# Kernel tuning notes

Measured on AMD Instinct MI355X. Metric: run time of the kernel, lower is better.

## Reference

```python
import jax, jax.numpy as jnp
import numpy as np

BETA = 0.25


def setup_inputs() -> dict:
    key = jax.random.key(0)
    k1, k2 = jax.random.split(key)
    z_e = jax.random.normal(k1, (16, 256, 2048), dtype=jnp.float32)   # [B, C, L]
    # nn.Embedding weight initialized uniform(-1, 1): [num_codewords, codebook_dim]
    emb = jax.random.uniform(k2, (2048, 256), dtype=jnp.float32, minval=-1.0, maxval=1.0)
    return {"z_e": z_e, "emb": emb}


def reference(z_e, emb):
    C = emb.shape[1]
    # Faithful to the torch code: permute(2,1,0) -> [L, C, B], then view(-1, C)
    z = jnp.transpose(z_e, (2, 1, 0))          # [L, C, B]
    flat = z.reshape(-1, C)                    # [N, C] where N = L*C*B / C
    d = (jnp.sum(flat * flat, axis=1, keepdims=True)
         + jnp.sum(emb * emb, axis=1)
         - 2.0 * flat @ emb.T)                 # [N, K]
    indices = jnp.argmin(d, axis=1)            # [N]
    quantized = emb[indices].reshape(z.shape)  # [L, C, B]
    sg = jax.lax.stop_gradient
    vq_loss = (jnp.mean((sg(quantized) - z) ** 2)
               + BETA * jnp.mean((quantized - sg(z)) ** 2))
    return quantized, indices, vq_loss
```

## Files before the change

### kernel.cpp

```cpp
#include <hip/hip_runtime.h>


#define ZE_CL   (256 * 2048)
#define NROWS   32768
#define KC      2048
#define DD      256
#define IDX_OFF 8388608
#define LOSS_OFF (8388608 + 32768)
#define D2 8e-3f

typedef __bf16 bf16x4 __attribute__((ext_vector_type(4)));
typedef __bf16 bf16x8 __attribute__((ext_vector_type(8)));
typedef float  f32x4  __attribute__((ext_vector_type(4)));

#define EN_OFF  0u
#define EH_OFF  8192u
#define EL_OFF  (EH_OFF + 1048576u)
#define AH_OFF  (EL_OFF + 1048576u)
#define AL_OFF  (AH_OFF + 16777216u)
#define CNT_OFF (AL_OFF + 16777216u)
#define LST_OFF (CNT_OFF + 16u)
#define WS_NEED (LST_OFF + 131072u)

static __device__ inline void gld_lds16(const void* g, void* l) {
    __builtin_amdgcn_global_load_lds(
        (const __attribute__((address_space(1))) void*)g,
        (__attribute__((address_space(3))) void*)l, 16, 0, 0);
}

__global__ void vq_prep_emb(const float* __restrict__ emb, float* __restrict__ enorm,
                            __bf16* __restrict__ Eh, __bf16* __restrict__ El) {
    int col = blockIdx.x * 256 + threadIdx.x;
    const float4* src = (const float4*)(emb + (size_t)col * DD);
    int t8 = col >> 8, g = (col >> 4) & 15, c = col & 15;
    float s = 0.f;
#pragma unroll
    for (int ch = 0; ch < 8; ++ch) {
#pragma unroll
        for (int q = 0; q < 4; ++q) {
            float4 v0 = src[ch * 8 + q * 2];
            float4 v1 = src[ch * 8 + q * 2 + 1];
            float f[8] = {v0.x, v0.y, v0.z, v0.w, v1.x, v1.y, v1.z, v1.w};
            bf16x8 h, l;
#pragma unroll
            for (int j = 0; j < 8; ++j) {
                h[j] = (__bf16)f[j];
                l[j] = (__bf16)(f[j] - (float)h[j]);
                s += f[j] * f[j];
            }
            size_t off = ((size_t)(t8 * 8 + ch) * 16384) + (size_t)(g * 1024 + q * 256 + c * 16);
            *(bf16x8*)((char*)Eh + off) = h;
            *(bf16x8*)((char*)El + off) = l;
        }
    }
    enorm[col] = s;
}

__global__ void vq_transpose_split(const float* __restrict__ ze, float* __restrict__ A,
                                   __bf16* __restrict__ Ah, __bf16* __restrict__ Al) {
    __shared__ float T[16 * 272];
    int tid = threadIdx.x;
    int m  = blockIdx.x & 15;
    int lt = blockIdx.x >> 4;
    int l0 = lt * 16;
#pragma unroll
    for (int it = 0; it < 4; ++it) {
        int p   = tid + it * 256;
        int b   = p >> 6;
        int clo = (p >> 2) & 15;
        int l4  = p & 3;
        const float* g = ze + (size_t)b * ZE_CL + (size_t)(m * 16 + clo) * 2048 + l0 + 4 * l4;
        float4 v = *(const float4*)g;
        int jp = 17 * clo + b;
        T[(4 * l4 + 0) * 272 + jp] = v.x;
        T[(4 * l4 + 1) * 272 + jp] = v.y;
        T[(4 * l4 + 2) * 272 + jp] = v.z;
        T[(4 * l4 + 3) * 272 + jp] = v.w;
    }
    __syncthreads();
#pragma unroll
    for (int it = 0; it < 4; ++it) {
        int p  = tid + it * 256;
        int ll = p >> 6;
        int c4 = p & 63;
        int j0 = 4 * c4;
        int base = ll * 272 + 17 * (j0 >> 4) + (j0 & 15);
        float4 v;
        v.x = T[base + 0]; v.y = T[base + 1]; v.z = T[base + 2]; v.w = T[base + 3];
        int n = (l0 + ll) * 16 + m;
        *(float4*)(A + (size_t)n * DD + j0) = v;
        if (Ah) {
            float a0 = -2.f * v.x, a1 = -2.f * v.y, a2 = -2.f * v.z, a3 = -2.f * v.w;
            bf16x4 h, l;
            h[0] = (__bf16)a0; l[0] = (__bf16)(a0 - (float)h[0]);
            h[1] = (__bf16)a1; l[1] = (__bf16)(a1 - (float)h[1]);
            h[2] = (__bf16)a2; l[2] = (__bf16)(a2 - (float)h[2]);
            h[3] = (__bf16)a3; l[3] = (__bf16)(a3 - (float)h[3]);
            int bn = n >> 6, mi = (n >> 4) & 3, r = n & 15;
            int ch = j0 >> 5, q = (j0 >> 3) & 3, hb = (j0 & 7) * 2;
            size_t off = (size_t)bn * 32768 + (size_t)((mi * 8 + ch) * 1024 + q * 256 + r * 16 + hb);
            *(bf16x4*)((char*)Ah + off) = h;
            *(bf16x4*)((char*)Al + off) = l;
        }
    }
}

__global__ __launch_bounds__(256, 2) void vq_main_mfma(
    const __bf16* __restrict__ Ah, const __bf16* __restrict__ Al,
    const __bf16* __restrict__ Eh, const __bf16* __restrict__ El,
    const float* __restrict__ enorm, const float* __restrict__ emb,
    float* out, int* __restrict__ rcount, int* __restrict__ rlist)
{
    __shared__ __align__(16) __bf16 sB[16384];
    __shared__ float sRv[256], sR2[256];
    __shared__ int   sRi[256];
    __shared__ int   sIdx[64], sFlag[64];
    __shared__ float wsum[4];

    const int tid  = threadIdx.x;
    const int wv   = tid >> 6;
    const int lane = tid & 63;
    const int l15  = lane & 15;
    const int quad = lane >> 4;
    const int n0   = blockIdx.x * 64;

    const char* AhB = (const char*)Ah + (size_t)blockIdx.x * 32768;
    const char* AlB = (const char*)Al + (size_t)blockIdx.x * 32768;

    float v1[16], v2[16]; int i1[16];
#pragma unroll
    for (int s = 0; s < 16; ++s) { v1[s] = 3.4e38f; v2[s] = 3.4e38f; i1[s] = 0; }

    for (int nt = 0; nt < 8; ++nt) {
        const char* EhT = (const char*)Eh + (size_t)nt * (8 * 16384);
        const char* ElT = (const char*)El + (size_t)nt * (8 * 16384);
        f32x4 acc[4][4];
#pragma unroll
        for (int a = 0; a < 4; ++a)
#pragma unroll
            for (int b = 0; b < 4; ++b) acc[a][b] = (f32x4){0.f, 0.f, 0.f, 0.f};

        for (int ch = 0; ch < 8; ++ch) {
            __syncthreads();
            {
                const char* srcH = EhT + ch * 16384;
                const char* srcL = ElT + ch * 16384;
#pragma unroll
                for (int it = 0; it < 4; ++it) {
                    int off = (it * 4 + wv) * 1024;
                    gld_lds16(srcH + off + lane * 16, (char*)sB + off);
                    gld_lds16(srcL + off + lane * 16, (char*)sB + 16384 + off);
                }
            }
            bf16x8 ah[4], al[4];
#pragma unroll
            for (int mi = 0; mi < 4; ++mi) {
                size_t off = (size_t)((mi * 8 + ch) * 1024 + quad * 256 + l15 * 16);
                ah[mi] = *(const bf16x8*)(AhB + off);
                al[mi] = *(const bf16x8*)(AlB + off);
            }
            __syncthreads();
            bf16x8 bh[4], bl[4];
#pragma unroll
            for (int nj = 0; nj < 4; ++nj) {
                int boff = (wv * 4 + nj) * 1024 + quad * 256 + l15 * 16;
                bh[nj] = *(const bf16x8*)((const char*)sB + boff);
                bl[nj] = *(const bf16x8*)((const char*)sB + 16384 + boff);
            }
#pragma unroll
            for (int mi = 0; mi < 4; ++mi)
#pragma unroll
                for (int nj = 0; nj < 4; ++nj)
                    acc[mi][nj] = __builtin_amdgcn_mfma_f32_16x16x32_bf16(ah[mi], bh[nj], acc[mi][nj], 0, 0, 0);
#pragma unroll
            for (int mi = 0; mi < 4; ++mi)
#pragma unroll
                for (int nj = 0; nj < 4; ++nj)
                    acc[mi][nj] = __builtin_amdgcn_mfma_f32_16x16x32_bf16(ah[mi], bl[nj], acc[mi][nj], 0, 0, 0);
#pragma unroll
            for (int mi = 0; mi < 4; ++mi)
#pragma unroll
                for (int nj = 0; nj < 4; ++nj)
                    acc[mi][nj] = __builtin_amdgcn_mfma_f32_16x16x32_bf16(al[mi], bh[nj], acc[mi][nj], 0, 0, 0);
        }
#pragma unroll
        for (int nj = 0; nj < 4; ++nj) {
            int k = nt * 256 + wv * 64 + nj * 16 + l15;
            float en = enorm[k];
#pragma unroll
            for (int mi = 0; mi < 4; ++mi)
#pragma unroll
                for (int r = 0; r < 4; ++r) {
                    float d = acc[mi][nj][r] + en;
                    int slot = mi * 4 + r;
                    float nv2 = fminf(v2[slot], fmaxf(v1[slot], d));
                    if (d < v1[slot]) i1[slot] = k;
                    v1[slot] = fminf(v1[slot], d);
                    v2[slot] = nv2;
                }
        }
    }

#pragma unroll
    for (int slot = 0; slot < 16; ++slot) {
        float a1 = v1[slot], a2 = v2[slot];
        int ai = i1[slot];
#pragma unroll
        for (int m = 1; m < 16; m <<= 1) {
            float b1 = __shfl_xor(a1, m, 64);
            float b2 = __shfl_xor(a2, m, 64);
            int bi = __shfl_xor(ai, m, 64);
            float n2 = fminf(fminf(a2, b2), fmaxf(a1, b1));
            if (b1 < a1) ai = bi;
            a1 = fminf(a1, b1);
            a2 = n2;
        }
        if (l15 == 0) {
            int row = (slot >> 2) * 16 + quad * 4 + (slot & 3);
            sRv[row * 4 + wv] = a1;
            sR2[row * 4 + wv] = a2;
            sRi[row * 4 + wv] = ai;
        }
    }
    __syncthreads();
    if (tid < 64) {
        float a1 = sRv[tid * 4], a2 = sR2[tid * 4];
        int ai = sRi[tid * 4];
#pragma unroll
        for (int w2 = 1; w2 < 4; ++w2) {
            float b1 = sRv[tid * 4 + w2], b2 = sR2[tid * 4 + w2];
            int bi = sRi[tid * 4 + w2];
            float n2 = fminf(fminf(a2, b2), fmaxf(a1, b1));
            if (b1 < a1) ai = bi;
            a1 = fminf(a1, b1);
            a2 = n2;
        }
        int fg = (a2 - a1 < D2) ? 1 : 0;
        sIdx[tid] = ai;
        sFlag[tid] = fg;
        out[IDX_OFF + n0 + tid] = (float)ai;
        if (fg) { int p = atomicAdd(rcount, 1); rlist[p] = n0 + tid; }
    }
    __syncthreads();

    float lacc = 0.f;
#pragma unroll
    for (int it = 0; it < 16; ++it) {
        int p = tid + it * 256;
        int r = p >> 6;
        int c4 = p & 63;
        if (!sFlag[r]) {
            int k = sIdx[r];
            size_t off = (size_t)(n0 + r) * DD + 4 * c4;
            float4 q = *(const float4*)(emb + (size_t)k * DD + 4 * c4);
            float4 a = *(const float4*)(out + off);
            float dx = q.x - a.x, dy = q.y - a.y, dz = q.z - a.z, dw = q.w - a.w;
            lacc += dx * dx + dy * dy + dz * dz + dw * dw;
            *(float4*)(out + off) = q;
        }
    }
#pragma unroll
    for (int off = 32; off > 0; off >>= 1) lacc += __shfl_down(lacc, off, 64);
    if ((tid & 63) == 0) wsum[tid >> 6] = lacc;
    __syncthreads();
    if (tid == 0) {
        float bs = wsum[0] + wsum[1] + wsum[2] + wsum[3];
        atomicAdd(out + LOSS_OFF, bs * (1.25f / 8388608.0f));
    }
}

__global__ void vq_rescore(const float* __restrict__ emb, const float* __restrict__ enorm,
                           float* out, const int* __restrict__ rcount,
                           const int* __restrict__ rlist) {
    __shared__ float sX[256];
    __shared__ float sV[256];
    __shared__ int   sK[256];
    __shared__ float sP[256];
    int cnt = *rcount;
    int tid = threadIdx.x;
    for (int li = blockIdx.x; li < cnt; li += gridDim.x) {
        int row = rlist[li];
        __syncthreads();
        sX[tid] = out[(size_t)row * DD + tid];
        __syncthreads();
        float bv = 3.4e38f; int bk = 0;
        for (int jj = 0; jj < 8; ++jj) {
            int k = jj * 256 + tid;
            const float4* e4 = (const float4*)(emb + (size_t)k * DD);
            float dot = 0.f;
#pragma unroll 8
            for (int d4 = 0; d4 < 64; ++d4) {
                float4 e = e4[d4];
                float4 x = *(const float4*)(sX + d4 * 4);
                dot += x.x * e.x + x.y * e.y + x.z * e.z + x.w * e.w;
            }
            float s = enorm[k] - 2.f * dot;
            if (s < bv) { bv = s; bk = k; }
        }
        sV[tid] = bv; sK[tid] = bk;
        __syncthreads();
#pragma unroll
        for (int s = 128; s > 0; s >>= 1) {
            if (tid < s) {
                float vo = sV[tid + s]; int ko = sK[tid + s];
                if (vo < sV[tid] || (vo == sV[tid] && ko < sK[tid])) { sV[tid] = vo; sK[tid] = ko; }
            }
            __syncthreads();
        }
        int k = sK[0];
        float x = sX[tid];
        float q = emb[(size_t)k * DD + tid];
        out[(size_t)row * DD + tid] = q;
        float d = q - x;
        sP[tid] = d * d;
        __syncthreads();
#pragma unroll
        for (int s = 128; s > 0; s >>= 1) {
            if (tid < s) sP[tid] += sP[tid + s];
            __syncthreads();
        }
        if (tid == 0) {
            out[IDX_OFF + row] = (float)k;
            atomicAdd(out + LOSS_OFF, sP[0] * (1.25f / 8388608.0f));
        }
    }
}

__global__ __launch_bounds__(256, 2) void vq_main_f32(const float* __restrict__ emb,
                                                      const float* __restrict__ enorm,
                                                      float* out) {
    const int SA = 68, SE = 68;
    __shared__ float smem[64 * 68 + 64 * 68];
    __shared__ int   sIdx[64];
    __shared__ float wsum[4];
    float* sA = smem;
    float* sEb = smem + 64 * SA;
    float* redv = sEb;
    int*   redi = (int*)(sEb + 64 * 16);
    int tid = threadIdx.x;
    int n0 = blockIdx.x * 64;
    int rg = tid & 15;
    int kg = tid >> 4;
    float minv[4]; int mini[4];
#pragma unroll
    for (int i = 0; i < 4; ++i) { minv[i] = 3.4e38f; mini[i] = 0; }
    const float* A = out;
    for (int kt = 0; kt < KC / 64; ++kt) {
        int k0 = kt * 64;
        float acc[4][4];
#pragma unroll
        for (int i = 0; i < 4; ++i)
#pragma unroll
            for (int j = 0; j < 4; ++j) acc[i][j] = 0.f;
        for (int dc = 0; dc < 4; ++dc) {
            int d0 = dc * 64;
            __syncthreads();
#pragma unroll
            for (int it = 0; it < 4; ++it) {
                int p = tid + it * 256, r = p >> 4, c4 = p & 15;
                *(float4*)(sA + r * SA + 4 * c4) =
                    *(const float4*)(A + (size_t)(n0 + r) * DD + d0 + 4 * c4);
            }
#pragma unroll
            for (int it = 0; it < 4; ++it) {
                int p = tid + it * 256, r = p >> 4, c4 = p & 15;
                *(float4*)(sEb + r * SE + 4 * c4) =
                    *(const float4*)(emb + (size_t)(k0 + r) * DD + d0 + 4 * c4);
            }
            __syncthreads();
#pragma unroll
            for (int d4 = 0; d4 < 16; ++d4) {
                float4 av[4], ev[4];
#pragma unroll
                for (int i = 0; i < 4; ++i) av[i] = *(const float4*)(sA + (rg + 16 * i) * SA + 4 * d4);
#pragma unroll
                for (int j = 0; j < 4; ++j) ev[j] = *(const float4*)(sEb + (kg + 16 * j) * SE + 4 * d4);
#pragma unroll
                for (int i = 0; i < 4; ++i)
#pragma unroll
                    for (int j = 0; j < 4; ++j)
                        acc[i][j] += av[i].x * ev[j].x + av[i].y * ev[j].y +
                                     av[i].z * ev[j].z + av[i].w * ev[j].w;
            }
        }
#pragma unroll
        for (int j = 0; j < 4; ++j) {
            int k = k0 + kg + 16 * j;
            float en = enorm[k];
#pragma unroll
            for (int i = 0; i < 4; ++i) {
                float s = en - 2.f * acc[i][j];
                if (s < minv[i]) { minv[i] = s; mini[i] = k; }
            }
        }
    }
    __syncthreads();
#pragma unroll
    for (int i = 0; i < 4; ++i) {
        int r = rg + 16 * i;
        redv[r * 16 + kg] = minv[i];
        redi[r * 16 + kg] = mini[i];
    }
    __syncthreads();
    if (tid < 64) {
        float bv = redv[tid * 16]; int bi = redi[tid * 16];
        for (int t = 1; t < 16; ++t) {
            float v = redv[tid * 16 + t]; int ii = redi[tid * 16 + t];
            if (v < bv || (v == bv && ii < bi)) { bv = v; bi = ii; }
        }
        sIdx[tid] = bi;
        out[IDX_OFF + n0 + tid] = (float)bi;
    }
    __syncthreads();
    float lacc = 0.f;
#pragma unroll
    for (int it = 0; it < 16; ++it) {
        int p = tid + it * 256, r = p >> 6, c4 = p & 63;
        int k = sIdx[r];
        size_t off = (size_t)(n0 + r) * DD + 4 * c4;
        float4 q = *(const float4*)(emb + (size_t)k * DD + 4 * c4);
        float4 a = *(const float4*)(out + off);
        float dx = q.x - a.x, dy = q.y - a.y, dz = q.z - a.z, dw = q.w - a.w;
        lacc += dx * dx + dy * dy + dz * dz + dw * dw;
        *(float4*)(out + off) = q;
    }
#pragma unroll
    for (int off = 32; off > 0; off >>= 1) lacc += __shfl_down(lacc, off, 64);
    if ((tid & 63) == 0) wsum[tid >> 6] = lacc;
    __syncthreads();
    if (tid == 0) {
        float bs = wsum[0] + wsum[1] + wsum[2] + wsum[3];
        atomicAdd(out + LOSS_OFF, bs * (1.25f / 8388608.0f));
    }
}

extern "C" void kernel_launch(void* const* d_in, const int* in_sizes, int n_in,
                              void* d_out, int out_size, void* d_ws, size_t ws_size,
                              hipStream_t stream) {
    (void)in_sizes; (void)n_in; (void)out_size;
    const float* ze  = (const float*)d_in[0];
    const float* emb = (const float*)d_in[1];
    float* out = (float*)d_out;
    char*  ws  = (char*)d_ws;
    float* enorm = (float*)(ws + EN_OFF);

    hipMemsetAsync((char*)d_out + (size_t)LOSS_OFF * 4, 0, 4, stream);

    if (ws_size >= (size_t)WS_NEED) {
        __bf16* Eh = (__bf16*)(ws + EH_OFF);
        __bf16* El = (__bf16*)(ws + EL_OFF);
        __bf16* Ah = (__bf16*)(ws + AH_OFF);
        __bf16* Al = (__bf16*)(ws + AL_OFF);
        int* rcount = (int*)(ws + CNT_OFF);
        int* rlist  = (int*)(ws + LST_OFF);
        hipMemsetAsync(ws + CNT_OFF, 0, 16, stream);
        vq_prep_emb<<<8, 256, 0, stream>>>(emb, enorm, Eh, El);
        vq_transpose_split<<<2048, 256, 0, stream>>>(ze, out, Ah, Al);
        vq_main_mfma<<<NROWS / 64, 256, 0, stream>>>(Ah, Al, Eh, El, enorm, emb, out, rcount, rlist);
        vq_rescore<<<64, 256, 0, stream>>>(emb, enorm, out, rcount, rlist);
    } else {
        {
        }
        vq_prep_emb<<<8, 256, 0, stream>>>(emb, enorm, (__bf16*)(ws + EH_OFF), (__bf16*)(ws + EH_OFF));
        vq_transpose_split<<<2048, 256, 0, stream>>>(ze, out, (__bf16*)0, (__bf16*)0);
        vq_main_f32<<<NROWS / 64, 256, 0, stream>>>(emb, enorm, out);
    }
}
```

Baseline: 309.4 us.

## Double-buffer codebook tiles in LDS and widen embedding prep parallelism

The main MFMA kernel now double-buffers the Eh/El codebook tiles in LDS. It prefetches the next tile with global_load_lds while the current tile is being multiplied, using explicit vmcnt waits and barriers in place of two __syncthreads per chunk. Enorm values are preloaded into registers and MFMA issue priority is raised with s_setprio. The embedding prep kernel splits each codeword across 8 threads and reduces the norm with shuffles, so it launches 64 blocks instead of 8. The trade-off is doubled LDS use and more registers, which may cut occupancy under the 2-block launch bound, and the hand-placed waitcnt logic is fragile.

```diff
diff --git a/kernel.cpp b/kernel.cpp
--- a/kernel.cpp
+++ b/kernel.cpp
@@ -30,30 +30,32 @@
 
 __global__ void vq_prep_emb(const float* __restrict__ emb, float* __restrict__ enorm,
                             __bf16* __restrict__ Eh, __bf16* __restrict__ El) {
-    int col = blockIdx.x * 256 + threadIdx.x;
+    int tid = threadIdx.x;
+    int col = blockIdx.x * 32 + (tid >> 3);
+    int ch  = tid & 7;
     const float4* src = (const float4*)(emb + (size_t)col * DD);
     int t8 = col >> 8, g = (col >> 4) & 15, c = col & 15;
     float s = 0.f;
 #pragma unroll
-    for (int ch = 0; ch < 8; ++ch) {
-#pragma unroll
-        for (int q = 0; q < 4; ++q) {
-            float4 v0 = src[ch * 8 + q * 2];
-            float4 v1 = src[ch * 8 + q * 2 + 1];
-            float f[8] = {v0.x, v0.y, v0.z, v0.w, v1.x, v1.y, v1.z, v1.w};
-            bf16x8 h, l;
-#pragma unroll
-            for (int j = 0; j < 8; ++j) {
-                h[j] = (__bf16)f[j];
-                l[j] = (__bf16)(f[j] - (float)h[j]);
-                s += f[j] * f[j];
-            }
-            size_t off = ((size_t)(t8 * 8 + ch) * 16384) + (size_t)(g * 1024 + q * 256 + c * 16);
-            *(bf16x8*)((char*)Eh + off) = h;
-            *(bf16x8*)((char*)El + off) = l;
-        }
-    }
-    enorm[col] = s;
+    for (int q = 0; q < 4; ++q) {
+        float4 v0 = src[ch * 8 + q * 2];
+        float4 v1 = src[ch * 8 + q * 2 + 1];
+        float f[8] = {v0.x, v0.y, v0.z, v0.w, v1.x, v1.y, v1.z, v1.w};
+        bf16x8 h, l;
+#pragma unroll
+        for (int j = 0; j < 8; ++j) {
+            h[j] = (__bf16)f[j];
+            l[j] = (__bf16)(f[j] - (float)h[j]);
+            s += f[j] * f[j];
+        }
+        size_t off = ((size_t)(t8 * 8 + ch) * 16384) + (size_t)(g * 1024 + q * 256 + c * 16);
+        *(bf16x8*)((char*)Eh + off) = h;
+        *(bf16x8*)((char*)El + off) = l;
+    }
+    s += __shfl_xor(s, 1, 64);
+    s += __shfl_xor(s, 2, 64);
+    s += __shfl_xor(s, 4, 64);
+    if (ch == 0) enorm[col] = s;
 }
 
 __global__ void vq_transpose_split(const float* __restrict__ ze, float* __restrict__ A,
@@ -111,7 +113,7 @@
     const float* __restrict__ enorm, const float* __restrict__ emb,
     float* out, int* __restrict__ rcount, int* __restrict__ rlist)
 {
-    __shared__ __align__(16) __bf16 sB[16384];
+    __shared__ __align__(16) __bf16 sB[2][16384];
     __shared__ float sRv[256], sR2[256];
     __shared__ int   sRi[256];
     __shared__ int   sIdx[64], sFlag[64];
@@ -131,27 +133,39 @@
 #pragma unroll
     for (int s = 0; s < 16; ++s) { v1[s] = 3.4e38f; v2[s] = 3.4e38f; i1[s] = 0; }
 
+    f32x4 acc[4][4];
+#pragma unroll
+    for (int a = 0; a < 4; ++a)
+#pragma unroll
+        for (int b = 0; b < 4; ++b) acc[a][b] = (f32x4){0.f, 0.f, 0.f, 0.f};
+
+    float enr[8][4];
+#pragma unroll
+    for (int t = 0; t < 8; ++t)
+#pragma unroll
+        for (int nj = 0; nj < 4; ++nj)
+            enr[t][nj] = enorm[t * 256 + wv * 64 + nj * 16 + l15];
+#pragma unroll
+    for (int t = 0; t < 8; ++t)
+#pragma unroll
+        for (int nj = 0; nj < 4; ++nj)
+            asm volatile("" :: "v"(enr[t][nj]));
+
+    {
+        char* dst = (char*)&sB[0][0];
+#pragma unroll
+        for (int it = 0; it < 4; ++it) {
+            int off = (it * 4 + wv) * 1024;
+            gld_lds16((const char*)Eh + off + lane * 16, dst + off);
+            gld_lds16((const char*)El + off + lane * 16, dst + 16384 + off);
+        }
+    }
+
+#pragma unroll
     for (int nt = 0; nt < 8; ++nt) {
-        const char* EhT = (const char*)Eh + (size_t)nt * (8 * 16384);
-        const char* ElT = (const char*)El + (size_t)nt * (8 * 16384);
-        f32x4 acc[4][4];
-#pragma unroll
-        for (int a = 0; a < 4; ++a)
-#pragma unroll
-            for (int b = 0; b < 4; ++b) acc[a][b] = (f32x4){0.f, 0.f, 0.f, 0.f};
-
+#pragma unroll 2
         for (int ch = 0; ch < 8; ++ch) {
-            __syncthreads();
-            {
-                const char* srcH = EhT + ch * 16384;
-                const char* srcL = ElT + ch * 16384;
-#pragma unroll
-                for (int it = 0; it < 4; ++it) {
-                    int off = (it * 4 + wv) * 1024;
-                    gld_lds16(srcH + off + lane * 16, (char*)sB + off);
-                    gld_lds16(srcL + off + lane * 16, (char*)sB + 16384 + off);
-                }
-            }
+            const int s = nt * 8 + ch;
             bf16x8 ah[4], al[4];
 #pragma unroll
             for (int mi = 0; mi < 4; ++mi) {
@@ -159,14 +173,35 @@
                 ah[mi] = *(const bf16x8*)(AhB + off);
                 al[mi] = *(const bf16x8*)(AlB + off);
             }
-            __syncthreads();
+            __builtin_amdgcn_sched_barrier(0);
+            if (s + 1 < 64) {
+                const int s1  = s + 1;
+                const int nt1 = s1 >> 3, ch1 = s1 & 7;
+                const char* srcH = (const char*)Eh + (size_t)nt1 * 131072 + (size_t)ch1 * 16384;
+                const char* srcL = (const char*)El + (size_t)nt1 * 131072 + (size_t)ch1 * 16384;
+                char* dst = (char*)&sB[s1 & 1][0];
+#pragma unroll
+                for (int it = 0; it < 4; ++it) {
+                    int off = (it * 4 + wv) * 1024;
+                    gld_lds16(srcH + off + lane * 16, dst + off);
+                    gld_lds16(srcL + off + lane * 16, dst + 16384 + off);
+                }
+                asm volatile("s_waitcnt vmcnt(16)" ::: "memory");
+            } else {
+                asm volatile("s_waitcnt vmcnt(8)" ::: "memory");
+            }
+            __builtin_amdgcn_s_barrier();
+            asm volatile("" ::: "memory");
+
+            const char* bufB = (const char*)&sB[ch & 1][0];
             bf16x8 bh[4], bl[4];
 #pragma unroll
             for (int nj = 0; nj < 4; ++nj) {
                 int boff = (wv * 4 + nj) * 1024 + quad * 256 + l15 * 16;
-                bh[nj] = *(const bf16x8*)((const char*)sB + boff);
-                bl[nj] = *(const bf16x8*)((const char*)sB + 16384 + boff);
-            }
+                bh[nj] = *(const bf16x8*)(bufB + boff);
+                bl[nj] = *(const bf16x8*)(bufB + 16384 + boff);
+            }
+            __builtin_amdgcn_s_setprio(1);
 #pragma unroll
             for (int mi = 0; mi < 4; ++mi)
 #pragma unroll
@@ -182,11 +217,15 @@
 #pragma unroll
                 for (int nj = 0; nj < 4; ++nj)
                     acc[mi][nj] = __builtin_amdgcn_mfma_f32_16x16x32_bf16(al[mi], bh[nj], acc[mi][nj], 0, 0, 0);
+            __builtin_amdgcn_s_setprio(0);
+            asm volatile("s_waitcnt lgkmcnt(0)" ::: "memory");
+            __builtin_amdgcn_s_barrier();
+            asm volatile("" ::: "memory");
         }
 #pragma unroll
         for (int nj = 0; nj < 4; ++nj) {
             int k = nt * 256 + wv * 64 + nj * 16 + l15;
-            float en = enorm[k];
+            float en = enr[nt][nj];
 #pragma unroll
             for (int mi = 0; mi < 4; ++mi)
 #pragma unroll
@@ -199,6 +238,10 @@
                     v2[slot] = nv2;
                 }
         }
+#pragma unroll
+        for (int a = 0; a < 4; ++a)
+#pragma unroll
+            for (int b = 0; b < 4; ++b) acc[a][b] = (f32x4){0.f, 0.f, 0.f, 0.f};
     }
 
 #pragma unroll
@@ -454,14 +497,12 @@
         int* rcount = (int*)(ws + CNT_OFF);
         int* rlist  = (int*)(ws + LST_OFF);
         hipMemsetAsync(ws + CNT_OFF, 0, 16, stream);
-        vq_prep_emb<<<8, 256, 0, stream>>>(emb, enorm, Eh, El);
+        vq_prep_emb<<<64, 256, 0, stream>>>(emb, enorm, Eh, El);
         vq_transpose_split<<<2048, 256, 0, stream>>>(ze, out, Ah, Al);
         vq_main_mfma<<<NROWS / 64, 256, 0, stream>>>(Ah, Al, Eh, El, enorm, emb, out, rcount, rlist);
         vq_rescore<<<64, 256, 0, stream>>>(emb, enorm, out, rcount, rlist);
     } else {
-        {
-        }
-        vq_prep_emb<<<8, 256, 0, stream>>>(emb, enorm, (__bf16*)(ws + EH_OFF), (__bf16*)(ws + EH_OFF));
+        vq_prep_emb<<<64, 256, 0, stream>>>(emb, enorm, (__bf16*)(ws + EH_OFF), (__bf16*)(ws + EH_OFF));
         vq_transpose_split<<<2048, 256, 0, stream>>>(ze, out, (__bf16*)0, (__bf16*)0);
         vq_main_f32<<<NROWS / 64, 256, 0, stream>>>(emb, enorm, out);
     }
```

Result: slower. 461.6 us (+49.2%).

## Load codebook fragments directly from global memory and parallelize embedding prep

Applied to the files above, without the earlier changes.

The main MFMA kernel stops staging codebook tiles through LDS with global_load_lds and two barriers per chunk. Each wave now loads its B fragments straight from global memory (relying on L2 reuse), and the chunk loop is unrolled by two. The embedding prep kernel spreads each codeword over 8 threads with a shuffle reduction for the norm, so it launches 64 blocks instead of 8. This removes synchronization and LDS traffic but adds redundant global and L2 reads of the codebook across blocks.

```diff
diff --git a/kernel.cpp b/kernel.cpp
--- a/kernel.cpp
+++ b/kernel.cpp
@@ -22,38 +22,34 @@
 #define LST_OFF (CNT_OFF + 16u)
 #define WS_NEED (LST_OFF + 131072u)
 
-static __device__ inline void gld_lds16(const void* g, void* l) {
-    __builtin_amdgcn_global_load_lds(
-        (const __attribute__((address_space(1))) void*)g,
-        (__attribute__((address_space(3))) void*)l, 16, 0, 0);
-}
-
 __global__ void vq_prep_emb(const float* __restrict__ emb, float* __restrict__ enorm,
                             __bf16* __restrict__ Eh, __bf16* __restrict__ El) {
-    int col = blockIdx.x * 256 + threadIdx.x;
+    int tid = threadIdx.x;
+    int col = blockIdx.x * 32 + (tid >> 3);
+    int ch  = tid & 7;
     const float4* src = (const float4*)(emb + (size_t)col * DD);
     int t8 = col >> 8, g = (col >> 4) & 15, c = col & 15;
     float s = 0.f;
 #pragma unroll
-    for (int ch = 0; ch < 8; ++ch) {
-#pragma unroll
-        for (int q = 0; q < 4; ++q) {
-            float4 v0 = src[ch * 8 + q * 2];
-            float4 v1 = src[ch * 8 + q * 2 + 1];
-            float f[8] = {v0.x, v0.y, v0.z, v0.w, v1.x, v1.y, v1.z, v1.w};
-            bf16x8 h, l;
-#pragma unroll
-            for (int j = 0; j < 8; ++j) {
-                h[j] = (__bf16)f[j];
-                l[j] = (__bf16)(f[j] - (float)h[j]);
-                s += f[j] * f[j];
-            }
-            size_t off = ((size_t)(t8 * 8 + ch) * 16384) + (size_t)(g * 1024 + q * 256 + c * 16);
-            *(bf16x8*)((char*)Eh + off) = h;
-            *(bf16x8*)((char*)El + off) = l;
-        }
-    }
-    enorm[col] = s;
+    for (int q = 0; q < 4; ++q) {
+        float4 v0 = src[ch * 8 + q * 2];
+        float4 v1 = src[ch * 8 + q * 2 + 1];
+        float f[8] = {v0.x, v0.y, v0.z, v0.w, v1.x, v1.y, v1.z, v1.w};
+        bf16x8 h, l;
+#pragma unroll
+        for (int j = 0; j < 8; ++j) {
+            h[j] = (__bf16)f[j];
+            l[j] = (__bf16)(f[j] - (float)h[j]);
+            s += f[j] * f[j];
+        }
+        size_t off = ((size_t)(t8 * 8 + ch) * 16384) + (size_t)(g * 1024 + q * 256 + c * 16);
+        *(bf16x8*)((char*)Eh + off) = h;
+        *(bf16x8*)((char*)El + off) = l;
+    }
+    s += __shfl_xor(s, 1, 64);
+    s += __shfl_xor(s, 2, 64);
+    s += __shfl_xor(s, 4, 64);
+    if (ch == 0) enorm[col] = s;
 }
 
 __global__ void vq_transpose_split(const float* __restrict__ ze, float* __restrict__ A,
@@ -111,7 +107,6 @@
     const float* __restrict__ enorm, const float* __restrict__ emb,
     float* out, int* __restrict__ rcount, int* __restrict__ rlist)
 {
-    __shared__ __align__(16) __bf16 sB[16384];
     __shared__ float sRv[256], sR2[256];
     __shared__ int   sRi[256];
     __shared__ int   sIdx[64], sFlag[64];
@@ -121,51 +116,40 @@
     const int wv   = tid >> 6;
     const int lane = tid & 63;
     const int l15  = lane & 15;
-    const int quad = lane >> 4;
     const int n0   = blockIdx.x * 64;
 
-    const char* AhB = (const char*)Ah + (size_t)blockIdx.x * 32768;
-    const char* AlB = (const char*)Al + (size_t)blockIdx.x * 32768;
+    const char* AhB = (const char*)Ah + (size_t)blockIdx.x * 32768 + (size_t)lane * 16;
+    const char* AlB = (const char*)Al + (size_t)blockIdx.x * 32768 + (size_t)lane * 16;
+    const char* EhW = (const char*)Eh + (size_t)(wv * 4) * 1024 + (size_t)lane * 16;
+    const char* ElW = (const char*)El + (size_t)(wv * 4) * 1024 + (size_t)lane * 16;
 
     float v1[16], v2[16]; int i1[16];
 #pragma unroll
     for (int s = 0; s < 16; ++s) { v1[s] = 3.4e38f; v2[s] = 3.4e38f; i1[s] = 0; }
 
     for (int nt = 0; nt < 8; ++nt) {
-        const char* EhT = (const char*)Eh + (size_t)nt * (8 * 16384);
-        const char* ElT = (const char*)El + (size_t)nt * (8 * 16384);
+        const char* EhT = EhW + (size_t)nt * 131072;
+        const char* ElT = ElW + (size_t)nt * 131072;
         f32x4 acc[4][4];
 #pragma unroll
         for (int a = 0; a < 4; ++a)
 #pragma unroll
             for (int b = 0; b < 4; ++b) acc[a][b] = (f32x4){0.f, 0.f, 0.f, 0.f};
 
+#pragma unroll 2
         for (int ch = 0; ch < 8; ++ch) {
-            __syncthreads();
-            {
-                const char* srcH = EhT + ch * 16384;
-                const char* srcL = ElT + ch * 16384;
-#pragma unroll
-                for (int it = 0; it < 4; ++it) {
-                    int off = (it * 4 + wv) * 1024;
-                    gld_lds16(srcH + off + lane * 16, (char*)sB + off);
-                    gld_lds16(srcL + off + lane * 16, (char*)sB + 16384 + off);
-                }
-            }
-            bf16x8 ah[4], al[4];
+            bf16x8 ah[4], al[4], bh[4], bl[4];
 #pragma unroll
             for (int mi = 0; mi < 4; ++mi) {
-                size_t off = (size_t)((mi * 8 + ch) * 1024 + quad * 256 + l15 * 16);
+                size_t off = (size_t)((mi * 8 + ch) * 1024);
                 ah[mi] = *(const bf16x8*)(AhB + off);
                 al[mi] = *(const bf16x8*)(AlB + off);
             }
-            __syncthreads();
-            bf16x8 bh[4], bl[4];
 #pragma unroll
             for (int nj = 0; nj < 4; ++nj) {
-                int boff = (wv * 4 + nj) * 1024 + quad * 256 + l15 * 16;
-                bh[nj] = *(const bf16x8*)((const char*)sB + boff);
-                bl[nj] = *(const bf16x8*)((const char*)sB + 16384 + boff);
+                size_t boff = (size_t)(ch * 16384 + nj * 1024);
+                bh[nj] = *(const bf16x8*)(EhT + boff);
+                bl[nj] = *(const bf16x8*)(ElT + boff);
             }
 #pragma unroll
             for (int mi = 0; mi < 4; ++mi)
@@ -201,6 +185,7 @@
         }
     }
 
+    const int quad = lane >> 4;
 #pragma unroll
     for (int slot = 0; slot < 16; ++slot) {
         float a1 = v1[slot], a2 = v2[slot];
@@ -454,14 +439,12 @@
         int* rcount = (int*)(ws + CNT_OFF);
         int* rlist  = (int*)(ws + LST_OFF);
         hipMemsetAsync(ws + CNT_OFF, 0, 16, stream);
-        vq_prep_emb<<<8, 256, 0, stream>>>(emb, enorm, Eh, El);
+        vq_prep_emb<<<64, 256, 0, stream>>>(emb, enorm, Eh, El);
         vq_transpose_split<<<2048, 256, 0, stream>>>(ze, out, Ah, Al);
         vq_main_mfma<<<NROWS / 64, 256, 0, stream>>>(Ah, Al, Eh, El, enorm, emb, out, rcount, rlist);
         vq_rescore<<<64, 256, 0, stream>>>(emb, enorm, out, rcount, rlist);
     } else {
-        {
-        }
-        vq_prep_emb<<<8, 256, 0, stream>>>(emb, enorm, (__bf16*)(ws + EH_OFF), (__bf16*)(ws + EH_OFF));
+        vq_prep_emb<<<64, 256, 0, stream>>>(emb, enorm, (__bf16*)(ws + EH_OFF), (__bf16*)(ws + EH_OFF));
         vq_transpose_split<<<2048, 256, 0, stream>>>(ze, out, (__bf16*)0, (__bf16*)0);
         vq_main_f32<<<NROWS / 64, 256, 0, stream>>>(emb, enorm, out);
     }
```

Result: no change. 304.6 us (-1.6%).
